# Kernel tuning notes

Hardware: AMD Instinct MI355X
Metric: run time of the kernel (lower is better)

Reference implementation:

```python
import jax, jax.numpy as jnp
import numpy as np

N = 100000
D = 256
E = 3200000


def setup_inputs() -> dict:
    key = jax.random.key(0)
    ks = jax.random.split(key, 8)
    x = jax.random.normal(ks[0], (N, D), dtype=jnp.float32)
    edge_index = jax.random.randint(ks[1], (2, E), 0, N, dtype=jnp.int64)
    s = 1.0 / np.sqrt(D)
    W_l = jax.random.uniform(ks[2], (D, D), dtype=jnp.float32, minval=-s, maxval=s)
    b_l = jax.random.uniform(ks[3], (D,), dtype=jnp.float32, minval=-s, maxval=s)
    W_r = jax.random.uniform(ks[4], (D, D), dtype=jnp.float32, minval=-s, maxval=s)
    ln_gamma = jnp.ones((D,), dtype=jnp.float32)
    ln_beta = jnp.zeros((D,), dtype=jnp.float32)
    return {"x": x, "edge_index": edge_index, "W_l": W_l, "b_l": b_l,
            "W_r": W_r, "ln_gamma": ln_gamma, "ln_beta": ln_beta}


def reference(x, edge_index, W_l, b_l, W_r, ln_gamma, ln_beta):
    src, dst = edge_index[0], edge_index[1]
    n = x.shape[0]
    # mean aggregation of neighbor (source) features onto destination nodes
    msg_sum = jax.ops.segment_sum(x[src], dst, num_segments=n)        # [N, D]
    deg = jax.ops.segment_sum(jnp.ones((src.shape[0],), x.dtype), dst,
                              num_segments=n)                          # [N]
    agg = msg_sum / jnp.maximum(deg, 1.0)[:, None]
    # SAGEConv: lin_l(agg) + lin_r(x)   (bias in lin_l only)
    f = agg @ W_l.T + b_l + x @ W_r.T
    # exact-erf GELU (torch F.gelu default)
    f = jax.nn.gelu(f, approximate=False)
    # LayerNorm over feature dim
    mu = jnp.mean(f, axis=-1, keepdims=True)
    var = jnp.var(f, axis=-1, keepdims=True)
    f = (f - mu) * jax.lax.rsqrt(var + 1e-5) * ln_gamma + ln_beta
    # dropout in eval mode = identity; residual add
    return f + x
```

## Files before the change

### kernel.cpp

```cpp
#include <hip/hip_runtime.h>

#define D 256
#define KDIM 512
#define BCAP 16384
#define EPB 8192
#define BM 128
#define BK 32
#define NT 16
#define DEPTH 3

typedef __bf16 bf16_t;
typedef bf16_t bf16x8 __attribute__((ext_vector_type(8)));
typedef bf16_t bf16x4 __attribute__((ext_vector_type(4)));
typedef float f32x4_t __attribute__((ext_vector_type(4)));
typedef float f32x2_t __attribute__((ext_vector_type(2)));

__device__ __forceinline__ void async_cp16(const void* g, void* l) {
    __builtin_amdgcn_global_load_lds(
        (const __attribute__((address_space(1))) unsigned int*)g,
        (__attribute__((address_space(3))) unsigned int*)l, 16, 0, 0);
}


__global__ __launch_bounds__(256) void k_scatter1(const int* __restrict__ eidx,
                                                  int* __restrict__ bcur,
                                                  int* __restrict__ staging, int E) {
    __shared__ int lhist[512];
    __shared__ int lcur[512];
    __shared__ int gbase[512];
    const int t = threadIdx.x;
    const int e0 = blockIdx.x * EPB;
    int e1 = e0 + EPB;
    if (e1 > E) e1 = E;

    lhist[t] = 0;
    lhist[t + 256] = 0;
    lcur[t] = 0;
    lcur[t + 256] = 0;
    __syncthreads();

    for (int e = e0 + t; e < e1; e += 256) {
        int d = eidx[E + e];
        atomicAdd(&lhist[d >> 8], 1);
    }
    __syncthreads();

#pragma unroll
    for (int b = t; b < 512; b += 256) {
        int c = lhist[b];
        gbase[b] = (c > 0) ? atomicAdd(&bcur[b * 16], c) : 0;
    }
    __syncthreads();

    for (int e = e0 + t; e < e1; e += 256) {
        int s = eidx[e];
        int d = eidx[E + e];
        int b = d >> 8;
        int pos = gbase[b] + atomicAdd(&lcur[b], 1);
        staging[(size_t)b * BCAP + pos] = ((d & 255) << 24) | s;
    }
}

__global__ __launch_bounds__(512) void k_bbase(const int* __restrict__ bcur,
                                               int* __restrict__ bbase,
                                               int* __restrict__ row_ptr,
                                               int B1, int N, int E) {
    __shared__ int sm[512];
    int t = threadIdx.x;
    int v = (t < B1) ? bcur[t * 16] : 0;
    sm[t] = v;
    __syncthreads();
    for (int off = 1; off < 512; off <<= 1) {
        int u = (t >= off) ? sm[t - off] : 0;
        __syncthreads();
        sm[t] += u;
        __syncthreads();
    }
    if (t < B1) bbase[t] = sm[t] - v;
    if (t == 0) row_ptr[N] = E;
}

__global__ __launch_bounds__(256) void k_bucket(const int* __restrict__ bcur,
                                                const int* __restrict__ bbase,
                                                const int* __restrict__ staging,
                                                int* __restrict__ edge_src,
                                                int* __restrict__ row_ptr, int N) {
    __shared__ int lhist[256];
    __shared__ int lscan[256];
    __shared__ int lcur[256];
    int b = blockIdx.x, t = threadIdx.x;
    int node_base = b << 8;
    int nn = N - node_base;
    if (nn > 256) nn = 256;
    int cnt = bcur[b * 16];
    int base = bbase[b];
    const int* stg = staging + (size_t)b * BCAP;

    lhist[t] = 0;
    __syncthreads();
    for (int i = t; i < cnt; i += 256)
        atomicAdd(&lhist[((unsigned)stg[i]) >> 24], 1);
    __syncthreads();
    int v = lhist[t];
    lscan[t] = v;
    __syncthreads();
    for (int off = 1; off < 256; off <<= 1) {
        int u = (t >= off) ? lscan[t - off] : 0;
        __syncthreads();
        lscan[t] += u;
        __syncthreads();
    }
    int excl = lscan[t] - v;
    if (t < nn) row_ptr[node_base + t] = base + excl;
    lscan[t] = excl;
    lcur[t] = 0;
    __syncthreads();
    for (int i = t; i < cnt; i += 256) {
        int w = stg[i];
        int ln = ((unsigned)w) >> 24;
        int src = w & 0xFFFFFF;
        int pos = base + lscan[ln] + atomicAdd(&lcur[ln], 1);
        edge_src[pos] = src;
    }
}


__global__ __launch_bounds__(256) void k_convx(const float* __restrict__ x,
                                               unsigned int* __restrict__ Xq,
                                               bf16_t* __restrict__ Xb,
                                               int total8) {
    int i = blockIdx.x * 256 + threadIdx.x;
    if (i >= total8) return;
    float4 v0 = *(const float4*)(x + (size_t)i * 8);
    float4 v1 = *(const float4*)(x + (size_t)i * 8 + 4);
    int w0 = 0, w1 = 0;
    w0 = __builtin_amdgcn_cvt_pk_fp8_f32(v0.x, v0.y, w0, false);
    w0 = __builtin_amdgcn_cvt_pk_fp8_f32(v0.z, v0.w, w0, true);
    w1 = __builtin_amdgcn_cvt_pk_fp8_f32(v1.x, v1.y, w1, false);
    w1 = __builtin_amdgcn_cvt_pk_fp8_f32(v1.z, v1.w, w1, true);
    uint2 o = {(unsigned)w0, (unsigned)w1};
    *(uint2*)(Xq + (size_t)i * 2) = o;
    bf16x8 ob = {(bf16_t)v0.x, (bf16_t)v0.y, (bf16_t)v0.z, (bf16_t)v0.w,
                 (bf16_t)v1.x, (bf16_t)v1.y, (bf16_t)v1.z, (bf16_t)v1.w};
    *(bf16x8*)(Xb + (size_t)i * 8) = ob;
}

__global__ __launch_bounds__(256) void k_convw(const float* __restrict__ Wl,
                                               const float* __restrict__ Wr,
                                               bf16_t* __restrict__ Wcat) {
    int i = blockIdx.x * 256 + threadIdx.x;
    if (i >= D * KDIM / 4) return;
    int o = i * 4;
    int j = o >> 9;
    int k = o & 511;
    const float* src = (k < D) ? (Wl + (size_t)j * D + k)
                               : (Wr + (size_t)j * D + (k - D));
    float4 v = *(const float4*)src;
    bf16x4 ov = {(bf16_t)v.x, (bf16_t)v.y, (bf16_t)v.z, (bf16_t)v.w};
    *(bf16x4*)(Wcat + o) = ov;
}


__global__ __launch_bounds__(256) void k_aggregate(const int* __restrict__ row_ptr,
                                                   const int* __restrict__ edge_src,
                                                   const unsigned int* __restrict__ Xq,
                                                   bf16_t* __restrict__ Agg, int N) {
    int wv = threadIdx.x >> 6;
    int lane = threadIdx.x & 63;
    int node = blockIdx.x * 4 + wv;
    if (node >= N) return;
    int g = lane >> 4;
    int c = lane & 15;
    int beg = row_ptr[node];
    int end = row_ptr[node + 1];

    float acc[16];
#pragma unroll
    for (int k = 0; k < 16; k++) acc[k] = 0.f;

#define ACC4(w, bidx)                                            \
    {                                                            \
        f32x2_t lo = __builtin_amdgcn_cvt_pk_f32_fp8((w), false);\
        f32x2_t hi = __builtin_amdgcn_cvt_pk_f32_fp8((w), true); \
        acc[(bidx) + 0] += lo[0];                                \
        acc[(bidx) + 1] += lo[1];                                \
        acc[(bidx) + 2] += hi[0];                                \
        acc[(bidx) + 3] += hi[1];                                \
    }

    for (int j = beg; j < end; j += 8) {
        int j0 = j + g, j1 = j + 4 + g;
        bool ok0 = j0 < end, ok1 = j1 < end;
        int s0 = edge_src[ok0 ? j0 : beg];
        int s1 = edge_src[ok1 ? j1 : beg];
        uint4 v0 = *(const uint4*)(Xq + (size_t)s0 * 64 + c * 4);
        uint4 v1 = *(const uint4*)(Xq + (size_t)s1 * 64 + c * 4);
        if (!ok0) { v0.x = 0; v0.y = 0; v0.z = 0; v0.w = 0; }
        if (!ok1) { v1.x = 0; v1.y = 0; v1.z = 0; v1.w = 0; }
        ACC4(v0.x, 0) ACC4(v0.y, 4) ACC4(v0.z, 8) ACC4(v0.w, 12)
        ACC4(v1.x, 0) ACC4(v1.y, 4) ACC4(v1.z, 8) ACC4(v1.w, 12)
    }
#undef ACC4

#pragma unroll
    for (int k = 0; k < 16; k++) {
        acc[k] += __shfl_xor(acc[k], 16, 64);
        acc[k] += __shfl_xor(acc[k], 32, 64);
    }
    int dg = end - beg;
    float inv = 1.0f / (float)(dg > 0 ? dg : 1);
    if (g == 0) {
        bf16x8 o0 = {(bf16_t)(acc[0] * inv), (bf16_t)(acc[1] * inv),
                     (bf16_t)(acc[2] * inv), (bf16_t)(acc[3] * inv),
                     (bf16_t)(acc[4] * inv), (bf16_t)(acc[5] * inv),
                     (bf16_t)(acc[6] * inv), (bf16_t)(acc[7] * inv)};
        bf16x8 o1 = {(bf16_t)(acc[8] * inv), (bf16_t)(acc[9] * inv),
                     (bf16_t)(acc[10] * inv), (bf16_t)(acc[11] * inv),
                     (bf16_t)(acc[12] * inv), (bf16_t)(acc[13] * inv),
                     (bf16_t)(acc[14] * inv), (bf16_t)(acc[15] * inv)};
        *(bf16x8*)(Agg + (size_t)node * D + c * 16) = o0;
        *(bf16x8*)(Agg + (size_t)node * D + c * 16 + 8) = o1;
    }
}


__global__ __launch_bounds__(512) void k_gemm(const bf16_t* __restrict__ Agg,
                                              const bf16_t* __restrict__ Xb,
                                              const bf16_t* __restrict__ Wcat,
                                              const float* __restrict__ x,
                                              const float* __restrict__ b_l,
                                              const float* __restrict__ gamma,
                                              const float* __restrict__ beta,
                                              float* __restrict__ out, int M) {
    __shared__ __align__(16) bf16_t As[DEPTH][BM * BK];
    __shared__ __align__(16) bf16_t Bs[DEPTH][D * BK];
    __shared__ float sm_s[4][BM];
    __shared__ float sm_q[4][BM];

    const int tid = threadIdx.x;
    const int lane = tid & 63;
    const int wid = tid >> 6;
    const int lr = lane & 15;
    const int lh = lane >> 4;
    const int wm = wid >> 2;
    const int wn = wid & 3;
    const int row0 = blockIdx.x * BM;

    const int sr = tid >> 2;
    const int sj = tid & 3;
    const int fA = (sr ^ (sr >> 2)) & 3;
    const int ar = (row0 + sr > M - 1) ? (M - 1) : (row0 + sr);
    const bf16_t* aggsrc = Agg + (size_t)ar * D + ((sj ^ fA) << 3);
    const bf16_t* xbsrc = Xb + (size_t)ar * D + ((sj ^ fA) << 3);
    const int rb1 = 128 + sr;
    const int fB1 = (rb1 ^ (rb1 >> 2)) & 3;
    const bf16_t* wsrc0 = Wcat + (size_t)sr * KDIM + ((sj ^ fA) << 3);
    const bf16_t* wsrc1 = Wcat + (size_t)rb1 * KDIM + ((sj ^ fB1) << 3);
    const int wbase8 = (tid & ~63) << 3;

#define STAGE(buf, k0)                                                         \
    do {                                                                       \
        async_cp16(((k0) < D) ? (aggsrc + (k0)) : (xbsrc + (k0) - D),          \
                   &As[buf][wbase8]);                                          \
        async_cp16(wsrc0 + (k0), &Bs[buf][wbase8]);                            \
        async_cp16(wsrc1 + (k0), &Bs[buf][4096 + wbase8]);                     \
    } while (0)

    f32x4_t acc[4][4];
#pragma unroll
    for (int i = 0; i < 4; i++)
#pragma unroll
        for (int j = 0; j < 4; j++) acc[i][j] = (f32x4_t){0.f, 0.f, 0.f, 0.f};

    STAGE(0, 0);
    STAGE(1, BK);

#pragma unroll
    for (int t = 0; t < NT; ++t) {
        if (t < NT - 1) {
            asm volatile("s_waitcnt vmcnt(3)" ::: "memory");
        } else {
            asm volatile("s_waitcnt vmcnt(0)" ::: "memory");
        }
        __builtin_amdgcn_s_barrier();
        __builtin_amdgcn_sched_barrier(0);
        if (t + 2 < NT) STAGE((t + 2) % DEPTH, (t + 2) * BK);

        const int cur = t % DEPTH;
        bf16x8 a[4], b[4];
#pragma unroll
        for (int mt = 0; mt < 4; mt++) {
            int ra = wm * 64 + mt * 16 + lr;
            int blk = lh ^ ((ra ^ (ra >> 2)) & 3);
            a[mt] = *(const bf16x8*)&As[cur][ra * BK + (blk << 3)];
        }
#pragma unroll
        for (int nt = 0; nt < 4; nt++) {
            int rbn = wn * 64 + nt * 16 + lr;
            int blk = lh ^ ((rbn ^ (rbn >> 2)) & 3);
            b[nt] = *(const bf16x8*)&Bs[cur][rbn * BK + (blk << 3)];
        }
#pragma unroll
        for (int mt = 0; mt < 4; mt++)
#pragma unroll
            for (int nt = 0; nt < 4; nt++)
                acc[mt][nt] = __builtin_amdgcn_mfma_f32_16x16x32_bf16(
                    a[mt], b[nt], acc[mt][nt], 0, 0, 0);
    }
#undef STAGE

    float bl[4], ga[4], be[4];
#pragma unroll
    for (int nt = 0; nt < 4; nt++) {
        int c = wn * 64 + nt * 16 + lr;
        bl[nt] = b_l[c];
        ga[nt] = gamma[c];
        be[nt] = beta[c];
    }

#pragma unroll
    for (int mt = 0; mt < 4; mt++) {
#pragma unroll
        for (int r = 0; r < 4; r++) {
            float s = 0.f, q = 0.f;
#pragma unroll
            for (int nt = 0; nt < 4; nt++) {
                float u = acc[mt][nt][r] + bl[nt];
                float ge = 0.5f * u * (1.0f + erff(u * 0.70710678118654752f));
                acc[mt][nt][r] = ge;
                s += ge;
                q += ge * ge;
            }
#pragma unroll
            for (int off = 8; off >= 1; off >>= 1) {
                s += __shfl_xor(s, off, 64);
                q += __shfl_xor(q, off, 64);
            }
            if (lr == 0) {
                int rl = wm * 64 + mt * 16 + lh * 4 + r;
                sm_s[wn][rl] = s;
                sm_q[wn][rl] = q;
            }
        }
    }
    __syncthreads();

#pragma unroll
    for (int mt = 0; mt < 4; mt++) {
#pragma unroll
        for (int r = 0; r < 4; r++) {
            int rl = wm * 64 + mt * 16 + lh * 4 + r;
            int m = row0 + rl;
            float S = sm_s[0][rl] + sm_s[1][rl] + sm_s[2][rl] + sm_s[3][rl];
            float Q = sm_q[0][rl] + sm_q[1][rl] + sm_q[2][rl] + sm_q[3][rl];
            float mean = S * (1.0f / 256.0f);
            float var = Q * (1.0f / 256.0f) - mean * mean;
            float rstd = rsqrtf(var + 1e-5f);
            if (m < M) {
#pragma unroll
                for (int nt = 0; nt < 4; nt++) {
                    int c = wn * 64 + nt * 16 + lr;
                    out[(size_t)m * D + c] =
                        (acc[mt][nt][r] - mean) * rstd * ga[nt] + be[nt] +
                        x[(size_t)m * D + c];
                }
            }
        }
    }
}


extern "C" void kernel_launch(void* const* d_in, const int* in_sizes, int n_in,
                              void* d_out, int out_size, void* d_ws, size_t ws_size,
                              hipStream_t stream) {
    const float* x = (const float*)d_in[0];
    const int* eidx = (const int*)d_in[1];
    const float* W_l = (const float*)d_in[2];
    const float* b_l = (const float*)d_in[3];
    const float* W_r = (const float*)d_in[4];
    const float* gamma = (const float*)d_in[5];
    const float* beta = (const float*)d_in[6];
    float* out = (float*)d_out;

    const int N = in_sizes[0] / D;
    const int E = in_sizes[1] / 2;
    const int B1 = (N + 255) >> 8;

    char* basep = (char*)d_ws;
    size_t off = 0;
    auto take = [&](size_t bytes) -> void* {
        void* r = basep + off;
        off += (bytes + 255) & ~(size_t)255;
        return r;
    };
    bf16_t* Agg = (bf16_t*)take((size_t)N * D * sizeof(bf16_t));
    bf16_t* Xb = (bf16_t*)take((size_t)N * D * sizeof(bf16_t));
    unsigned int* Xq = (unsigned int*)take((size_t)N * (D / 4) * 4);
    int* edge_src = (int*)take((size_t)E * sizeof(int));
    bf16_t* Wcat = (bf16_t*)take((size_t)D * KDIM * sizeof(bf16_t));
    int* row_ptr = (int*)take((size_t)(N + 1) * sizeof(int));
    int* bcur = (int*)take((size_t)B1 * 16 * sizeof(int));
    int* bbase = (int*)take((size_t)B1 * sizeof(int));
    int* staging = (int*)Agg;

    hipMemsetAsync(bcur, 0, (size_t)B1 * 16 * sizeof(int), stream);

    k_scatter1<<<(E + EPB - 1) / EPB, 256, 0, stream>>>(eidx, bcur, staging, E);
    k_bbase<<<1, 512, 0, stream>>>(bcur, bbase, row_ptr, B1, N, E);
    k_bucket<<<B1, 256, 0, stream>>>(bcur, bbase, staging, edge_src, row_ptr, N);

    k_convx<<<(N * (D / 8) + 255) / 256, 256, 0, stream>>>(x, Xq, Xb, N * (D / 8));
    k_convw<<<(D * KDIM / 4 + 255) / 256, 256, 0, stream>>>(W_l, W_r, Wcat);

    k_aggregate<<<(N + 3) / 4, 256, 0, stream>>>(row_ptr, edge_src, Xq, Agg, N);

    k_gemm<<<(N + BM - 1) / BM, 512, 0, stream>>>(Agg, Xb, Wcat, x, b_l, gamma,
                                                  beta, out, N);
}
```

Before: 337.9 us.

## Fuse neighbor aggregation into GEMM epilogue kernel via LDS-resident aggregate tile

Merges the aggregation kernel and the GEMM into one kernel: each block aggregates 64 nodes into a swizzled LDS tile, runs the first K half of the MFMA GEMM, then loads the bf16 x tile into the same LDS for the second half. The intermediate Agg buffer round trip through HBM is removed, and the residual reads bf16 x from LDS instead of fp32 x from global. The trade-offs are lower residual precision, W fragments read straight from global/L2 with no LDS pipelining, and a smaller tile.

```diff
diff --git a/kernel.cpp b/kernel.cpp
--- a/kernel.cpp
+++ b/kernel.cpp
@@ -4,10 +4,7 @@
 #define KDIM 512
 #define BCAP 16384
 #define EPB 8192
-#define BM 128
-#define BK 32
-#define NT 16
-#define DEPTH 3
+#define BM 64
 
 typedef __bf16 bf16_t;
 typedef bf16_t bf16x8 __attribute__((ext_vector_type(8)));
@@ -142,7 +139,10 @@
     *(uint2*)(Xq + (size_t)i * 2) = o;
     bf16x8 ob = {(bf16_t)v0.x, (bf16_t)v0.y, (bf16_t)v0.z, (bf16_t)v0.w,
                  (bf16_t)v1.x, (bf16_t)v1.y, (bf16_t)v1.z, (bf16_t)v1.w};
-    *(bf16x8*)(Xb + (size_t)i * 8) = ob;
+    int row = i >> 5;
+    int blk = i & 31;
+    int dblk = blk ^ ((row & 7) << 2);
+    *(bf16x8*)(Xb + (size_t)row * D + dblk * 8) = ob;
 }
 
 __global__ __launch_bounds__(256) void k_convw(const float* __restrict__ Wl,
@@ -161,22 +161,35 @@
 }
 
 
-__global__ __launch_bounds__(256) void k_aggregate(const int* __restrict__ row_ptr,
-                                                   const int* __restrict__ edge_src,
-                                                   const unsigned int* __restrict__ Xq,
-                                                   bf16_t* __restrict__ Agg, int N) {
-    int wv = threadIdx.x >> 6;
-    int lane = threadIdx.x & 63;
-    int node = blockIdx.x * 4 + wv;
-    if (node >= N) return;
-    int g = lane >> 4;
-    int c = lane & 15;
-    int beg = row_ptr[node];
-    int end = row_ptr[node + 1];
-
-    float acc[16];
-#pragma unroll
-    for (int k = 0; k < 16; k++) acc[k] = 0.f;
+__global__ __launch_bounds__(256, 4) void k_fused(
+        const int* __restrict__ row_ptr, const int* __restrict__ edge_src,
+        const unsigned int* __restrict__ Xq, const bf16_t* __restrict__ Xb,
+        const bf16_t* __restrict__ Wcat, const float* __restrict__ b_l,
+        const float* __restrict__ gamma, const float* __restrict__ beta,
+        float* __restrict__ out, int M) {
+    __shared__ __align__(16) bf16_t A_lds[BM * D];
+    __shared__ float sm_s[4][BM];
+    __shared__ float sm_q[4][BM];
+
+    const int tid = threadIdx.x;
+    const int lane = tid & 63;
+    const int wid = tid >> 6;
+    const int lr = lane & 15;
+    const int lh = lane >> 4;
+    const int g = lane >> 4;
+    const int c16 = lane & 15;
+    const int row0 = blockIdx.x * BM;
+
+    for (int rr = 0; rr < 16; ++rr) {
+        int rl = wid * 16 + rr;
+        int node = row0 + rl;
+        if (node > M - 1) node = M - 1;
+        int beg = row_ptr[node];
+        int end = row_ptr[node + 1];
+
+        float acc[16];
+#pragma unroll
+        for (int k = 0; k < 16; k++) acc[k] = 0.f;
 
 #define ACC4(w, bidx)                                            \
     {                                                            \
@@ -187,84 +200,42 @@
         acc[(bidx) + 2] += hi[0];                                \
         acc[(bidx) + 3] += hi[1];                                \
     }
-
-    for (int j = beg; j < end; j += 8) {
-        int j0 = j + g, j1 = j + 4 + g;
-        bool ok0 = j0 < end, ok1 = j1 < end;
-        int s0 = edge_src[ok0 ? j0 : beg];
-        int s1 = edge_src[ok1 ? j1 : beg];
-        uint4 v0 = *(const uint4*)(Xq + (size_t)s0 * 64 + c * 4);
-        uint4 v1 = *(const uint4*)(Xq + (size_t)s1 * 64 + c * 4);
-        if (!ok0) { v0.x = 0; v0.y = 0; v0.z = 0; v0.w = 0; }
-        if (!ok1) { v1.x = 0; v1.y = 0; v1.z = 0; v1.w = 0; }
-        ACC4(v0.x, 0) ACC4(v0.y, 4) ACC4(v0.z, 8) ACC4(v0.w, 12)
-        ACC4(v1.x, 0) ACC4(v1.y, 4) ACC4(v1.z, 8) ACC4(v1.w, 12)
-    }
+        for (int j = beg; j < end; j += 8) {
+            int j0 = j + g, j1 = j + 4 + g;
+            bool ok0 = j0 < end, ok1 = j1 < end;
+            int s0 = edge_src[ok0 ? j0 : beg];
+            int s1 = edge_src[ok1 ? j1 : beg];
+            uint4 v0 = *(const uint4*)(Xq + (size_t)s0 * 64 + c16 * 4);
+            uint4 v1 = *(const uint4*)(Xq + (size_t)s1 * 64 + c16 * 4);
+            if (!ok0) { v0.x = 0; v0.y = 0; v0.z = 0; v0.w = 0; }
+            if (!ok1) { v1.x = 0; v1.y = 0; v1.z = 0; v1.w = 0; }
+            ACC4(v0.x, 0) ACC4(v0.y, 4) ACC4(v0.z, 8) ACC4(v0.w, 12)
+            ACC4(v1.x, 0) ACC4(v1.y, 4) ACC4(v1.z, 8) ACC4(v1.w, 12)
+        }
 #undef ACC4
 
 #pragma unroll
-    for (int k = 0; k < 16; k++) {
-        acc[k] += __shfl_xor(acc[k], 16, 64);
-        acc[k] += __shfl_xor(acc[k], 32, 64);
-    }
-    int dg = end - beg;
-    float inv = 1.0f / (float)(dg > 0 ? dg : 1);
-    if (g == 0) {
-        bf16x8 o0 = {(bf16_t)(acc[0] * inv), (bf16_t)(acc[1] * inv),
-                     (bf16_t)(acc[2] * inv), (bf16_t)(acc[3] * inv),
-                     (bf16_t)(acc[4] * inv), (bf16_t)(acc[5] * inv),
-                     (bf16_t)(acc[6] * inv), (bf16_t)(acc[7] * inv)};
-        bf16x8 o1 = {(bf16_t)(acc[8] * inv), (bf16_t)(acc[9] * inv),
-                     (bf16_t)(acc[10] * inv), (bf16_t)(acc[11] * inv),
-                     (bf16_t)(acc[12] * inv), (bf16_t)(acc[13] * inv),
-                     (bf16_t)(acc[14] * inv), (bf16_t)(acc[15] * inv)};
-        *(bf16x8*)(Agg + (size_t)node * D + c * 16) = o0;
-        *(bf16x8*)(Agg + (size_t)node * D + c * 16 + 8) = o1;
-    }
-}
-
-
-__global__ __launch_bounds__(512) void k_gemm(const bf16_t* __restrict__ Agg,
-                                              const bf16_t* __restrict__ Xb,
-                                              const bf16_t* __restrict__ Wcat,
-                                              const float* __restrict__ x,
-                                              const float* __restrict__ b_l,
-                                              const float* __restrict__ gamma,
-                                              const float* __restrict__ beta,
-                                              float* __restrict__ out, int M) {
-    __shared__ __align__(16) bf16_t As[DEPTH][BM * BK];
-    __shared__ __align__(16) bf16_t Bs[DEPTH][D * BK];
-    __shared__ float sm_s[4][BM];
-    __shared__ float sm_q[4][BM];
-
-    const int tid = threadIdx.x;
-    const int lane = tid & 63;
-    const int wid = tid >> 6;
-    const int lr = lane & 15;
-    const int lh = lane >> 4;
-    const int wm = wid >> 2;
-    const int wn = wid & 3;
-    const int row0 = blockIdx.x * BM;
-
-    const int sr = tid >> 2;
-    const int sj = tid & 3;
-    const int fA = (sr ^ (sr >> 2)) & 3;
-    const int ar = (row0 + sr > M - 1) ? (M - 1) : (row0 + sr);
-    const bf16_t* aggsrc = Agg + (size_t)ar * D + ((sj ^ fA) << 3);
-    const bf16_t* xbsrc = Xb + (size_t)ar * D + ((sj ^ fA) << 3);
-    const int rb1 = 128 + sr;
-    const int fB1 = (rb1 ^ (rb1 >> 2)) & 3;
-    const bf16_t* wsrc0 = Wcat + (size_t)sr * KDIM + ((sj ^ fA) << 3);
-    const bf16_t* wsrc1 = Wcat + (size_t)rb1 * KDIM + ((sj ^ fB1) << 3);
-    const int wbase8 = (tid & ~63) << 3;
-
-#define STAGE(buf, k0)                                                         \
-    do {                                                                       \
-        async_cp16(((k0) < D) ? (aggsrc + (k0)) : (xbsrc + (k0) - D),          \
-                   &As[buf][wbase8]);                                          \
-        async_cp16(wsrc0 + (k0), &Bs[buf][wbase8]);                            \
-        async_cp16(wsrc1 + (k0), &Bs[buf][4096 + wbase8]);                     \
-    } while (0)
+        for (int k = 0; k < 16; k++) {
+            acc[k] += __shfl_xor(acc[k], 16, 64);
+            acc[k] += __shfl_xor(acc[k], 32, 64);
+        }
+        int dg = end - beg;
+        float inv = 1.0f / (float)(dg > 0 ? dg : 1);
+        if (g == 0) {
+            int f = (rl & 7) << 2;
+            bf16x8 o0 = {(bf16_t)(acc[0] * inv), (bf16_t)(acc[1] * inv),
+                         (bf16_t)(acc[2] * inv), (bf16_t)(acc[3] * inv),
+                         (bf16_t)(acc[4] * inv), (bf16_t)(acc[5] * inv),
+                         (bf16_t)(acc[6] * inv), (bf16_t)(acc[7] * inv)};
+            bf16x8 o1 = {(bf16_t)(acc[8] * inv), (bf16_t)(acc[9] * inv),
+                         (bf16_t)(acc[10] * inv), (bf16_t)(acc[11] * inv),
+                         (bf16_t)(acc[12] * inv), (bf16_t)(acc[13] * inv),
+                         (bf16_t)(acc[14] * inv), (bf16_t)(acc[15] * inv)};
+            *(bf16x8*)&A_lds[rl * D + ((2 * c16) ^ f) * 8] = o0;
+            *(bf16x8*)&A_lds[rl * D + ((2 * c16 + 1) ^ f) * 8] = o1;
+        }
+    }
+    __syncthreads();
 
     f32x4_t acc[4][4];
 #pragma unroll
@@ -272,47 +243,44 @@
 #pragma unroll
         for (int j = 0; j < 4; j++) acc[i][j] = (f32x4_t){0.f, 0.f, 0.f, 0.f};
 
-    STAGE(0, 0);
-    STAGE(1, BK);
-
-#pragma unroll
-    for (int t = 0; t < NT; ++t) {
-        if (t < NT - 1) {
-            asm volatile("s_waitcnt vmcnt(3)" ::: "memory");
-        } else {
-            asm volatile("s_waitcnt vmcnt(0)" ::: "memory");
-        }
-        __builtin_amdgcn_s_barrier();
-        __builtin_amdgcn_sched_barrier(0);
-        if (t + 2 < NT) STAGE((t + 2) % DEPTH, (t + 2) * BK);
-
-        const int cur = t % DEPTH;
-        bf16x8 a[4], b[4];
-#pragma unroll
-        for (int mt = 0; mt < 4; mt++) {
-            int ra = wm * 64 + mt * 16 + lr;
-            int blk = lh ^ ((ra ^ (ra >> 2)) & 3);
-            a[mt] = *(const bf16x8*)&As[cur][ra * BK + (blk << 3)];
-        }
-#pragma unroll
-        for (int nt = 0; nt < 4; nt++) {
-            int rbn = wn * 64 + nt * 16 + lr;
-            int blk = lh ^ ((rbn ^ (rbn >> 2)) & 3);
-            b[nt] = *(const bf16x8*)&Bs[cur][rbn * BK + (blk << 3)];
-        }
-#pragma unroll
-        for (int mt = 0; mt < 4; mt++)
-#pragma unroll
-            for (int nt = 0; nt < 4; nt++)
-                acc[mt][nt] = __builtin_amdgcn_mfma_f32_16x16x32_bf16(
-                    a[mt], b[nt], acc[mt][nt], 0, 0, 0);
-    }
-#undef STAGE
+    const bf16_t* wb = Wcat + (size_t)(wid * 64 + lr) * KDIM;
+
+#define KHALF(koff)                                                            \
+    _Pragma("unroll 2") for (int k0 = 0; k0 < 256; k0 += 32) {                 \
+        int kk = k0 + lh * 8;                                                  \
+        bf16x8 a[4], b[4];                                                     \
+        _Pragma("unroll") for (int mt = 0; mt < 4; mt++) {                     \
+            int ra = mt * 16 + lr;                                             \
+            int blk = ((k0 >> 3) + lh) ^ ((ra & 7) << 2);                      \
+            a[mt] = *(const bf16x8*)&A_lds[ra * D + blk * 8];                  \
+        }                                                                      \
+        _Pragma("unroll") for (int nt = 0; nt < 4; nt++)                       \
+            b[nt] = *(const bf16x8*)(wb + (size_t)nt * 16 * KDIM + (koff) + kk);\
+        _Pragma("unroll") for (int mt = 0; mt < 4; mt++)                       \
+            _Pragma("unroll") for (int nt = 0; nt < 4; nt++)                   \
+                acc[mt][nt] = __builtin_amdgcn_mfma_f32_16x16x32_bf16(         \
+                    a[mt], b[nt], acc[mt][nt], 0, 0, 0);                       \
+    }
+
+    KHALF(0)
+
+    __syncthreads();
+    {
+        const char* src = (const char*)(Xb + (size_t)row0 * D) + wid * 8192;
+        char* dst = (char*)A_lds + wid * 8192;
+#pragma unroll
+        for (int o = 0; o < 8; ++o)
+            async_cp16(src + o * 1024 + lane * 16, dst + o * 1024 + lane * 16);
+    }
+    __syncthreads();
+
+    KHALF(256)
+#undef KHALF
 
     float bl[4], ga[4], be[4];
 #pragma unroll
     for (int nt = 0; nt < 4; nt++) {
-        int c = wn * 64 + nt * 16 + lr;
+        int c = wid * 64 + nt * 16 + lr;
         bl[nt] = b_l[c];
         ga[nt] = gamma[c];
         be[nt] = beta[c];
@@ -337,9 +305,9 @@
                 q += __shfl_xor(q, off, 64);
             }
             if (lr == 0) {
-                int rl = wm * 64 + mt * 16 + lh * 4 + r;
-                sm_s[wn][rl] = s;
-                sm_q[wn][rl] = q;
+                int rl = mt * 16 + lh * 4 + r;
+                sm_s[wid][rl] = s;
+                sm_q[wid][rl] = q;
             }
         }
     }
@@ -349,7 +317,7 @@
     for (int mt = 0; mt < 4; mt++) {
 #pragma unroll
         for (int r = 0; r < 4; r++) {
-            int rl = wm * 64 + mt * 16 + lh * 4 + r;
+            int rl = mt * 16 + lh * 4 + r;
             int m = row0 + rl;
             float S = sm_s[0][rl] + sm_s[1][rl] + sm_s[2][rl] + sm_s[3][rl];
             float Q = sm_q[0][rl] + sm_q[1][rl] + sm_q[2][rl] + sm_q[3][rl];
@@ -357,12 +325,14 @@
             float var = Q * (1.0f / 256.0f) - mean * mean;
             float rstd = rsqrtf(var + 1e-5f);
             if (m < M) {
+                int f = (rl & 7) << 2;
 #pragma unroll
                 for (int nt = 0; nt < 4; nt++) {
-                    int c = wn * 64 + nt * 16 + lr;
+                    int c = wid * 64 + nt * 16 + lr;
+                    float res = (float)A_lds[rl * D + (((c >> 3) ^ f) << 3) +
+                                             (c & 7)];
                     out[(size_t)m * D + c] =
-                        (acc[mt][nt][r] - mean) * rstd * ga[nt] + be[nt] +
-                        x[(size_t)m * D + c];
+                        (acc[mt][nt][r] - mean) * rstd * ga[nt] + be[nt] + res;
                 }
             }
         }
@@ -393,7 +363,6 @@
         off += (bytes + 255) & ~(size_t)255;
         return r;
     };
-    bf16_t* Agg = (bf16_t*)take((size_t)N * D * sizeof(bf16_t));
     bf16_t* Xb = (bf16_t*)take((size_t)N * D * sizeof(bf16_t));
     unsigned int* Xq = (unsigned int*)take((size_t)N * (D / 4) * 4);
     int* edge_src = (int*)take((size_t)E * sizeof(int));
@@ -401,7 +370,7 @@
     int* row_ptr = (int*)take((size_t)(N + 1) * sizeof(int));
     int* bcur = (int*)take((size_t)B1 * 16 * sizeof(int));
     int* bbase = (int*)take((size_t)B1 * sizeof(int));
-    int* staging = (int*)Agg;
+    int* staging = (int*)Xb;
 
     hipMemsetAsync(bcur, 0, (size_t)B1 * 16 * sizeof(int), stream);
 
@@ -412,8 +381,6 @@
     k_convx<<<(N * (D / 8) + 255) / 256, 256, 0, stream>>>(x, Xq, Xb, N * (D / 8));
     k_convw<<<(D * KDIM / 4 + 255) / 256, 256, 0, stream>>>(W_l, W_r, Wcat);
 
-    k_aggregate<<<(N + 3) / 4, 256, 0, stream>>>(row_ptr, edge_src, Xq, Agg, N);
-
-    k_gemm<<<(N + BM - 1) / BM, 512, 0, stream>>>(Agg, Xb, Wcat, x, b_l, gamma,
-                                                  beta, out, N);
-}
+    k_fused<<<(N + BM - 1) / BM, 256, 0, stream>>>(row_ptr, edge_src, Xq, Xb,
+                                                   Wcat, b_l, gamma, beta, out, N);
+}
```

Result: slower. 348.4 us (+3.1%).

## Restructure fused GEMM: full-K A tile in LDS, B from global, bf16 residual

Applied to the files above, without the earlier changes.

Replaces the triple-buffered K-pipelined GEMM (128-row tiles, 512 threads) with 64-row tiles. The entire 64x512 A tile (Agg and Xb concatenated) is loaded into LDS once with an XOR swizzle. Each of the 4 waves reads its 64 output columns of the weight matrix directly from global or L2 instead of staging them through LDS. The epilogue takes the residual from the bf16 Xb copy already in LDS rather than reading fp32 x from global, which saves memory traffic but lowers residual precision. Smaller blocks and fewer barriers aim at better occupancy and less synchronisation, at the cost of repeated uncached-in-LDS weight loads.

```diff
diff --git a/kernel.cpp b/kernel.cpp
--- a/kernel.cpp
+++ b/kernel.cpp
@@ -4,10 +4,7 @@
 #define KDIM 512
 #define BCAP 16384
 #define EPB 8192
-#define BM 128
-#define BK 32
-#define NT 16
-#define DEPTH 3
+#define BM 64
 
 typedef __bf16 bf16_t;
 typedef bf16_t bf16x8 __attribute__((ext_vector_type(8)));
@@ -224,16 +221,12 @@
 }
 
 
-__global__ __launch_bounds__(512) void k_gemm(const bf16_t* __restrict__ Agg,
-                                              const bf16_t* __restrict__ Xb,
-                                              const bf16_t* __restrict__ Wcat,
-                                              const float* __restrict__ x,
-                                              const float* __restrict__ b_l,
-                                              const float* __restrict__ gamma,
-                                              const float* __restrict__ beta,
-                                              float* __restrict__ out, int M) {
-    __shared__ __align__(16) bf16_t As[DEPTH][BM * BK];
-    __shared__ __align__(16) bf16_t Bs[DEPTH][D * BK];
+__global__ __launch_bounds__(256) void k_gemm(
+        const bf16_t* __restrict__ Agg, const bf16_t* __restrict__ Xb,
+        const bf16_t* __restrict__ Wcat, const float* __restrict__ b_l,
+        const float* __restrict__ gamma, const float* __restrict__ beta,
+        float* __restrict__ out, int M) {
+    __shared__ __align__(16) bf16_t A_lds[BM * KDIM];
     __shared__ float sm_s[4][BM];
     __shared__ float sm_q[4][BM];
 
@@ -242,29 +235,19 @@
     const int wid = tid >> 6;
     const int lr = lane & 15;
     const int lh = lane >> 4;
-    const int wm = wid >> 2;
-    const int wn = wid & 3;
     const int row0 = blockIdx.x * BM;
 
-    const int sr = tid >> 2;
-    const int sj = tid & 3;
-    const int fA = (sr ^ (sr >> 2)) & 3;
-    const int ar = (row0 + sr > M - 1) ? (M - 1) : (row0 + sr);
-    const bf16_t* aggsrc = Agg + (size_t)ar * D + ((sj ^ fA) << 3);
-    const bf16_t* xbsrc = Xb + (size_t)ar * D + ((sj ^ fA) << 3);
-    const int rb1 = 128 + sr;
-    const int fB1 = (rb1 ^ (rb1 >> 2)) & 3;
-    const bf16_t* wsrc0 = Wcat + (size_t)sr * KDIM + ((sj ^ fA) << 3);
-    const bf16_t* wsrc1 = Wcat + (size_t)rb1 * KDIM + ((sj ^ fB1) << 3);
-    const int wbase8 = (tid & ~63) << 3;
-
-#define STAGE(buf, k0)                                                         \
-    do {                                                                       \
-        async_cp16(((k0) < D) ? (aggsrc + (k0)) : (xbsrc + (k0) - D),          \
-                   &As[buf][wbase8]);                                          \
-        async_cp16(wsrc0 + (k0), &Bs[buf][wbase8]);                            \
-        async_cp16(wsrc1 + (k0), &Bs[buf][4096 + wbase8]);                     \
-    } while (0)
+#pragma unroll
+    for (int o = 0; o < 16; ++o) {
+        int r = o * 4 + wid;
+        int gr = row0 + r;
+        if (gr > M - 1) gr = M - 1;
+        int lb = lane ^ (r & 7);
+        const bf16_t* src = (lane < 32) ? (Agg + (size_t)gr * D + lb * 8)
+                                        : (Xb + (size_t)gr * D + (lb - 32) * 8);
+        async_cp16(src, &A_lds[r * KDIM]);
+    }
+    __syncthreads();
 
     f32x4_t acc[4][4];
 #pragma unroll
@@ -272,34 +255,20 @@
 #pragma unroll
         for (int j = 0; j < 4; j++) acc[i][j] = (f32x4_t){0.f, 0.f, 0.f, 0.f};
 
-    STAGE(0, 0);
-    STAGE(1, BK);
-
-#pragma unroll
-    for (int t = 0; t < NT; ++t) {
-        if (t < NT - 1) {
-            asm volatile("s_waitcnt vmcnt(3)" ::: "memory");
-        } else {
-            asm volatile("s_waitcnt vmcnt(0)" ::: "memory");
+    const bf16_t* wb = Wcat + (size_t)(wid * 64 + lr) * KDIM;
+
+#pragma unroll 4
+    for (int k0 = 0; k0 < KDIM; k0 += 32) {
+        const int kb = (k0 >> 3) + lh;
+        bf16x8 a[4], b[4];
+#pragma unroll
+        for (int mt = 0; mt < 4; mt++) {
+            int ra = mt * 16 + lr;
+            a[mt] = *(const bf16x8*)&A_lds[ra * KDIM + ((kb ^ (ra & 7)) << 3)];
         }
-        __builtin_amdgcn_s_barrier();
-        __builtin_amdgcn_sched_barrier(0);
-        if (t + 2 < NT) STAGE((t + 2) % DEPTH, (t + 2) * BK);
-
-        const int cur = t % DEPTH;
-        bf16x8 a[4], b[4];
-#pragma unroll
-        for (int mt = 0; mt < 4; mt++) {
-            int ra = wm * 64 + mt * 16 + lr;
-            int blk = lh ^ ((ra ^ (ra >> 2)) & 3);
-            a[mt] = *(const bf16x8*)&As[cur][ra * BK + (blk << 3)];
-        }
-#pragma unroll
-        for (int nt = 0; nt < 4; nt++) {
-            int rbn = wn * 64 + nt * 16 + lr;
-            int blk = lh ^ ((rbn ^ (rbn >> 2)) & 3);
-            b[nt] = *(const bf16x8*)&Bs[cur][rbn * BK + (blk << 3)];
-        }
+#pragma unroll
+        for (int nt = 0; nt < 4; nt++)
+            b[nt] = *(const bf16x8*)(wb + (size_t)nt * 16 * KDIM + k0 + lh * 8);
 #pragma unroll
         for (int mt = 0; mt < 4; mt++)
 #pragma unroll
@@ -307,12 +276,11 @@
                 acc[mt][nt] = __builtin_amdgcn_mfma_f32_16x16x32_bf16(
                     a[mt], b[nt], acc[mt][nt], 0, 0, 0);
     }
-#undef STAGE
 
     float bl[4], ga[4], be[4];
 #pragma unroll
     for (int nt = 0; nt < 4; nt++) {
-        int c = wn * 64 + nt * 16 + lr;
+        int c = wid * 64 + nt * 16 + lr;
         bl[nt] = b_l[c];
         ga[nt] = gamma[c];
         be[nt] = beta[c];
@@ -337,9 +305,9 @@
                 q += __shfl_xor(q, off, 64);
             }
             if (lr == 0) {
-                int rl = wm * 64 + mt * 16 + lh * 4 + r;
-                sm_s[wn][rl] = s;
-                sm_q[wn][rl] = q;
+                int rl = mt * 16 + lh * 4 + r;
+                sm_s[wid][rl] = s;
+                sm_q[wid][rl] = q;
             }
         }
     }
@@ -349,7 +317,7 @@
     for (int mt = 0; mt < 4; mt++) {
 #pragma unroll
         for (int r = 0; r < 4; r++) {
-            int rl = wm * 64 + mt * 16 + lh * 4 + r;
+            int rl = mt * 16 + lh * 4 + r;
             int m = row0 + rl;
             float S = sm_s[0][rl] + sm_s[1][rl] + sm_s[2][rl] + sm_s[3][rl];
             float Q = sm_q[0][rl] + sm_q[1][rl] + sm_q[2][rl] + sm_q[3][rl];
@@ -359,10 +327,11 @@
             if (m < M) {
 #pragma unroll
                 for (int nt = 0; nt < 4; nt++) {
-                    int c = wn * 64 + nt * 16 + lr;
+                    int c = wid * 64 + nt * 16 + lr;
+                    int pb = (32 + (c >> 3)) ^ (rl & 7);
+                    float res = (float)A_lds[rl * KDIM + pb * 8 + (c & 7)];
                     out[(size_t)m * D + c] =
-                        (acc[mt][nt][r] - mean) * rstd * ga[nt] + be[nt] +
-                        x[(size_t)m * D + c];
+                        (acc[mt][nt][r] - mean) * rstd * ga[nt] + be[nt] + res;
                 }
             }
         }
@@ -414,6 +383,6 @@
 
     k_aggregate<<<(N + 3) / 4, 256, 0, stream>>>(row_ptr, edge_src, Xq, Agg, N);
 
-    k_gemm<<<(N + BM - 1) / BM, 512, 0, stream>>>(Agg, Xb, Wcat, x, b_l, gamma,
+    k_gemm<<<(N + BM - 1) / BM, 256, 0, stream>>>(Agg, Xb, Wcat, b_l, gamma,
                                                   beta, out, N);
 }
```

New measurement: 355.3 us. 1.05x slower.
